# Performance work log

Measured on AMD Instinct MI355X. Metric: run time of the kernel, lower is better.

Reference implementation:

```python
import jax, jax.numpy as jnp
import numpy as np

NUM_NODES = 200000
NUM_LAYERS = 3
EMBED_DIM = 64
NUM_EDGES = 3200000
NUM_PAIRS = 1000000


def setup_inputs() -> dict:
    key = jax.random.key(0)
    k1, k2, k3 = jax.random.split(key, 3)
    emb = jax.random.normal(k1, (NUM_NODES, EMBED_DIM), dtype=jnp.float32)
    alpha = jnp.ones((NUM_LAYERS + 1,), dtype=jnp.float32) * (1.0 / (NUM_LAYERS + 1))
    edge_index = jax.random.randint(k2, (2, NUM_EDGES), 0, NUM_NODES, dtype=jnp.int32)
    edge_label_index = jax.random.randint(k3, (2, NUM_PAIRS), 0, NUM_NODES, dtype=jnp.int32)
    return {"emb": emb, "alpha": alpha, "edge_index": edge_index,
            "edge_label_index": edge_label_index}


def reference(emb, alpha, edge_index, edge_label_index):
    row, col = edge_index[0], edge_index[1]  # source -> target
    # symmetric normalization (gcn_norm without self-loops, as in LGConv)
    ones = jnp.ones((row.shape[0],), dtype=emb.dtype)
    deg = jax.ops.segment_sum(ones, col, num_segments=NUM_NODES)
    dinv = jnp.where(deg > 0, jax.lax.rsqrt(jnp.maximum(deg, 1.0)), 0.0)
    norm = dinv[row] * dinv[col]  # [E]

    x = emb
    out = x * alpha[0]
    for l in range(NUM_LAYERS):
        # gather messages from sources, scale by norm, scatter-add into targets
        msgs = x[row] * norm[:, None]                      # [E, D]
        x = jax.ops.segment_sum(msgs, col, num_segments=NUM_NODES)  # [N, D]
        out = out + x * alpha[l + 1]

    src = out[edge_label_index[0]]  # [P, D]
    dst = out[edge_label_index[1]]  # [P, D]
    return jnp.sum(src * dst, axis=-1)  # [P]
```

## Files before the change

### kernel.cpp

```cpp
#include <hip/hip_runtime.h>
#include <hip/hip_fp16.h>

#define N_NODES 200000
#define N_EDGES 3200000
#define N_PAIRS 1000000
#define DIM 64
#define CAP 48
#define NPB 256
#define NB 782
#define BKTCAP 5120
#define BSTRIDE 16

#define CBITS 11
#define NBC 98
#define BKTCAPA 34816
#define CHUNKA 4096
#define NBLKA ((N_EDGES + CHUNKA - 1) / CHUNKA)
#define BUFB 4400

__global__ void partA_kernel(const int* __restrict__ row, const int* __restrict__ col,
                             int* __restrict__ bktcntA, unsigned* __restrict__ stagingA, int E) {
    __shared__ unsigned buf[CHUNKA];
    __shared__ int cntA[128], offA[128];
    __shared__ int curA[NBC], baseA[NBC];
    int tid = threadIdx.x;
    for (int i = tid; i < 128; i += 256) cntA[i] = 0;
    __syncthreads();
    int start = blockIdx.x * CHUNKA;
    unsigned pk[16];
    int bk[16];
    #pragma unroll
    for (int k = 0; k < 16; ++k) {
        int e = start + k * 256 + tid;
        if (e < E) {
            int c = col[e];
            int r = row[e];
            pk[k] = ((unsigned)(c & 2047) << 18) | (unsigned)r;
            bk[k] = c >> CBITS;
            atomicAdd(&cntA[bk[k]], 1);
        } else bk[k] = -1;
    }
    __syncthreads();
    if (tid < 128) offA[tid] = cntA[tid];
    __syncthreads();
    for (int d = 1; d < 128; d <<= 1) {
        int v = 0;
        if (tid < 128 && tid >= d) v = offA[tid - d];
        __syncthreads();
        if (tid < 128) offA[tid] += v;
        __syncthreads();
    }
    if (tid < NBC) {
        int x = offA[tid] - cntA[tid];
        curA[tid] = x;
        offA[tid] = x;
        baseA[tid] = (cntA[tid] > 0) ? atomicAdd(&bktcntA[tid * BSTRIDE], cntA[tid]) : 0;
    }
    __syncthreads();
    #pragma unroll
    for (int k = 0; k < 16; ++k) {
        if (bk[k] >= 0) {
            int p = atomicAdd(&curA[bk[k]], 1);
            buf[p] = pk[k];
        }
    }
    __syncthreads();
    for (int b = 0; b < NBC; ++b) {
        int n = cntA[b];
        if (n == 0) continue;
        int base = baseA[b];
        if (base + n > BKTCAPA) n = max(0, BKTCAPA - base);
        unsigned* dst = stagingA + (size_t)b * BKTCAPA + base;
        const int o = offA[b];
        for (int i = tid; i < n; i += 256) dst[i] = buf[o + i];
    }
}

__global__ void partB_kernel(const unsigned* __restrict__ stagingA, const int* __restrict__ bktcntA,
                             int* __restrict__ bktcntB, unsigned* __restrict__ stagingB) {
    __shared__ unsigned buf[BUFB];
    __shared__ int cntB[8], offB[8], curB[8], baseB[8];
    int bc = blockIdx.x >> 3;
    int s  = blockIdx.x & 7;
    int tid = threadIdx.x;
    if (tid < 8) cntB[tid] = 0;
    __syncthreads();
    int cnt = min(bktcntA[bc * BSTRIDE], BKTCAPA);
    int slice = (cnt + 7) >> 3;
    int lo = s * slice;
    int hi = min(lo + slice, cnt);
    int n = max(hi - lo, 0);
    const unsigned* src = stagingA + (size_t)bc * BKTCAPA + lo;
    for (int i = tid; i < n; i += 256) atomicAdd(&cntB[src[i] >> 26], 1);
    __syncthreads();
    if (tid == 0) {
        int a = 0;
        for (int b = 0; b < 8; ++b) { offB[b] = a; a += cntB[b]; }
    }
    __syncthreads();
    if (tid < 8) {
        curB[tid] = offB[tid];
        baseB[tid] = (cntB[tid] > 0) ? atomicAdd(&bktcntB[(bc * 8 + tid) * BSTRIDE], cntB[tid]) : 0;
    }
    __syncthreads();
    for (int i = tid; i < n; i += 256) {
        unsigned e = src[i];
        int fb = e >> 26;
        int p = atomicAdd(&curB[fb], 1);
        buf[p] = e & 0x3FFFFFFu;
    }
    __syncthreads();
    for (int b = 0; b < 8; ++b) {
        int m = cntB[b];
        if (m == 0) continue;
        int base = baseB[b];
        if (base + m > BKTCAP) m = max(0, BKTCAP - base);
        unsigned* dst = stagingB + (size_t)(bc * 8 + b) * BKTCAP + base;
        const int o = offB[b];
        for (int i = tid; i < m; i += 256) dst[i] = buf[o + i];
    }
}

__global__ void build_kernel(const unsigned* __restrict__ staging, const int* __restrict__ bktcnt,
                             int* __restrict__ srcrow, int* __restrict__ deg,
                             float* __restrict__ dinv, int N) {
    __shared__ int tile[NPB * CAP];
    __shared__ int cur[NPB];
    int b = blockIdx.x;
    for (int i = threadIdx.x; i < NPB; i += 256) cur[i] = 0;
    __syncthreads();
    int cnt = min(bktcnt[b * BSTRIDE], BKTCAP);
    const unsigned* st = staging + (size_t)b * BKTCAP;
    for (int i = threadIdx.x; i < cnt; i += 256) {
        unsigned packed = st[i];
        int r = packed & 0x3FFFF;
        int cl = packed >> 18;
        int p = atomicAdd(&cur[cl], 1);
        if (p < CAP) tile[cl * CAP + p] = r;
    }
    __syncthreads();
    int nodeBase = b * NPB;
    int nvalid = min(NPB, N - nodeBase);
    for (int i = threadIdx.x; i < nvalid; i += 256) {
        int d = min(cur[i], CAP);
        deg[nodeBase + i] = d;
        dinv[nodeBase + i] = (d > 0) ? rsqrtf((float)d) : 0.0f;
    }
    int tot = nvalid * CAP;
    int* dst = srcrow + (size_t)nodeBase * CAP;
    for (int i = threadIdx.x; i < tot; i += 256) dst[i] = tile[i];
}

__global__ void ewpack_kernel(unsigned int* __restrict__ ew, const int* __restrict__ deg,
                              int total) {
    int s = blockIdx.x * blockDim.x + threadIdx.x;
    if (s >= total) return;
    int n = s / CAP;
    int l = s - n * CAP;
    unsigned int e = 0;
    if (l < deg[n]) {
        int r = (int)ew[s];
        e = (unsigned int)r | ((unsigned int)deg[r] << 18);
    }
    ew[s] = e;
}

__global__ void convert_kernel(const float2* __restrict__ x, __half2* __restrict__ y, int n2) {
    int i = blockIdx.x * blockDim.x + threadIdx.x;
    if (i < n2) {
        float2 v = x[i];
        y[i] = __floats2half2_rn(v.x, v.y);
    }
}

__device__ __forceinline__ float2 h2f(unsigned int u) {
    __half2 h = *(__half2*)&u;
    return __half22float2(h);
}

__global__ void prop_kernel(const uint2* __restrict__ x, const unsigned int* __restrict__ ew,
                            const int* __restrict__ deg, const float* __restrict__ dinv,
                            uint2* __restrict__ xn, int N) {
    __shared__ int2 lds[4][CAP];
    int wv = threadIdx.x >> 6;
    int n = blockIdx.x * 4 + wv;
    int l = threadIdx.x & 63;
    int q = l & 15;
    int quarter = l >> 4;
    int cnt = deg[n];
    if (l < CAP) {
        unsigned int e = ew[(unsigned int)n * CAP + l];
        int id = e & 0x3FFFF;
        int dr = e >> 18;
        float w = dr ? rsqrtf((float)dr) : 0.0f;
        lds[wv][l] = make_int2(id, __float_as_int(w));
    }
    __syncthreads();
    float a0 = 0.f, a1 = 0.f, a2 = 0.f, a3 = 0.f;
    int trips = (cnt + 3) >> 2;
    #pragma unroll 4
    for (int k = 0; k < trips; ++k) {
        int2 e = lds[wv][k * 4 + quarter];
        float w = __int_as_float(e.y);
        uint2 pix = x[(unsigned int)e.x * 16u + q];
        float2 flo = h2f(pix.x);
        float2 fhi = h2f(pix.y);
        a0 += flo.x * w; a1 += flo.y * w;
        a2 += fhi.x * w; a3 += fhi.y * w;
    }
    a0 += __shfl_xor(a0, 16, 64); a1 += __shfl_xor(a1, 16, 64);
    a2 += __shfl_xor(a2, 16, 64); a3 += __shfl_xor(a3, 16, 64);
    a0 += __shfl_xor(a0, 32, 64); a1 += __shfl_xor(a1, 32, 64);
    a2 += __shfl_xor(a2, 32, 64); a3 += __shfl_xor(a3, 32, 64);
    float dn = dinv[n];
    if (quarter == 0) {
        __half2 o01 = __floats2half2_rn(a0 * dn, a1 * dn);
        __half2 o23 = __floats2half2_rn(a2 * dn, a3 * dn);
        uint2 out;
        out.x = *(unsigned int*)&o01;
        out.y = *(unsigned int*)&o23;
        xn[(unsigned int)n * 16u + q] = out;
    }
}

__global__ void prop_final_kernel(const uint2* __restrict__ x, const unsigned int* __restrict__ ew,
                                  const int* __restrict__ deg, const float* __restrict__ dinv,
                                  const uint2* __restrict__ h0, const uint2* __restrict__ h1,
                                  const float* __restrict__ alpha,
                                  uint2* __restrict__ outh, int N) {
    __shared__ int2 lds[4][CAP];
    int wv = threadIdx.x >> 6;
    int n = blockIdx.x * 4 + wv;
    int l = threadIdx.x & 63;
    int q = l & 15;
    int quarter = l >> 4;
    int cnt = deg[n];
    if (l < CAP) {
        unsigned int e = ew[(unsigned int)n * CAP + l];
        int id = e & 0x3FFFF;
        int dr = e >> 18;
        float w = dr ? rsqrtf((float)dr) : 0.0f;
        lds[wv][l] = make_int2(id, __float_as_int(w));
    }
    __syncthreads();
    float a0 = 0.f, a1 = 0.f, a2 = 0.f, a3 = 0.f;
    int trips = (cnt + 3) >> 2;
    #pragma unroll 4
    for (int k = 0; k < trips; ++k) {
        int2 e = lds[wv][k * 4 + quarter];
        float w = __int_as_float(e.y);
        uint2 pix = x[(unsigned int)e.x * 16u + q];
        float2 flo = h2f(pix.x);
        float2 fhi = h2f(pix.y);
        a0 += flo.x * w; a1 += flo.y * w;
        a2 += fhi.x * w; a3 += fhi.y * w;
    }
    a0 += __shfl_xor(a0, 16, 64); a1 += __shfl_xor(a1, 16, 64);
    a2 += __shfl_xor(a2, 16, 64); a3 += __shfl_xor(a3, 16, 64);
    a0 += __shfl_xor(a0, 32, 64); a1 += __shfl_xor(a1, 32, 64);
    a2 += __shfl_xor(a2, 32, 64); a3 += __shfl_xor(a3, 32, 64);
    float dn = dinv[n];
    if (quarter == 0) {
        float al0 = alpha[0], al1 = alpha[1], al2 = alpha[2], al3 = alpha[3];
        unsigned int idx = (unsigned int)n * 16u + q;
        uint2 p0 = h0[idx];
        uint2 p1 = h1[idx];
        uint2 p2 = x[idx];
        float2 f0l = h2f(p0.x), f0h = h2f(p0.y);
        float2 f1l = h2f(p1.x), f1h = h2f(p1.y);
        float2 f2l = h2f(p2.x), f2h = h2f(p2.y);
        float r0 = al0 * f0l.x + al1 * f1l.x + al2 * f2l.x + al3 * (a0 * dn);
        float r1 = al0 * f0l.y + al1 * f1l.y + al2 * f2l.y + al3 * (a1 * dn);
        float r2 = al0 * f0h.x + al1 * f1h.x + al2 * f2h.x + al3 * (a2 * dn);
        float r3 = al0 * f0h.y + al1 * f1h.y + al2 * f2h.y + al3 * (a3 * dn);
        __half2 o01 = __floats2half2_rn(r0, r1);
        __half2 o23 = __floats2half2_rn(r2, r3);
        uint2 out;
        out.x = *(unsigned int*)&o01;
        out.y = *(unsigned int*)&o23;
        outh[idx] = out;
    }
}

__global__ void dot_kernel(const uint2* __restrict__ outh, const int* __restrict__ pa,
                           const int* __restrict__ pb, float* __restrict__ res, int P) {
    int t = blockIdx.x * blockDim.x + threadIdx.x;
    int g = t >> 4;
    int l = threadIdx.x & 15;
    int half = P >> 1;
    if (g >= half) return;
    int p0 = g, p1 = g + half;
    int a0 = pa[p0], b0 = pb[p0];
    int a1 = pa[p1], b1 = pb[p1];
    uint2 ua0 = outh[(size_t)a0 * 16 + l];
    uint2 ub0 = outh[(size_t)b0 * 16 + l];
    uint2 ua1 = outh[(size_t)a1 * 16 + l];
    uint2 ub1 = outh[(size_t)b1 * 16 + l];
    float2 fx0 = h2f(ua0.x), fx1 = h2f(ua0.y);
    float2 fy0 = h2f(ub0.x), fy1 = h2f(ub0.y);
    float s0 = fx0.x * fy0.x + fx0.y * fy0.y + fx1.x * fy1.x + fx1.y * fy1.y;
    float2 fu0 = h2f(ua1.x), fu1 = h2f(ua1.y);
    float2 fv0 = h2f(ub1.x), fv1 = h2f(ub1.y);
    float s1 = fu0.x * fv0.x + fu0.y * fv0.y + fu1.x * fv1.x + fu1.y * fv1.y;
    s0 += __shfl_xor(s0, 1, 64);
    s1 += __shfl_xor(s1, 1, 64);
    s0 += __shfl_xor(s0, 2, 64);
    s1 += __shfl_xor(s1, 2, 64);
    s0 += __shfl_xor(s0, 4, 64);
    s1 += __shfl_xor(s1, 4, 64);
    s0 += __shfl_xor(s0, 8, 64);
    s1 += __shfl_xor(s1, 8, 64);
    if (l == 0) {
        res[p0] = s0;
        res[p1] = s1;
    }
}

extern "C" void kernel_launch(void* const* d_in, const int* in_sizes, int n_in,
                              void* d_out, int out_size, void* d_ws, size_t ws_size,
                              hipStream_t stream) {
    const float* emb   = (const float*)d_in[0];
    const float* alpha = (const float*)d_in[1];
    const int*   ei    = (const int*)d_in[2];
    const int*   eli   = (const int*)d_in[3];
    const int* row = ei;
    const int* col = ei + N_EDGES;
    const int* pa  = eli;
    const int* pb  = eli + N_PAIRS;
    float* res = (float*)d_out;

    const size_t hfeat_bytes = (size_t)N_NODES * DIM * sizeof(__half);
    char* ws = (char*)d_ws;
    size_t off = 0;
    auto alloc = [&](size_t bytes) {
        void* p = ws + off;
        off += (bytes + 255) & ~(size_t)255;
        return p;
    };
    int*      bktcntA  = (int*)alloc((size_t)NBC * BSTRIDE * sizeof(int));
    int*      bktcntB  = (int*)alloc((size_t)NB * BSTRIDE * sizeof(int));
    unsigned* stagingA = (unsigned*)alloc((size_t)NBC * BKTCAPA * sizeof(unsigned));
    unsigned* stagingB = (unsigned*)alloc((size_t)NB * BKTCAP * sizeof(unsigned));
    int*      srcrow   = (int*)alloc((size_t)N_NODES * CAP * sizeof(int));
    int*      deg      = (int*)alloc((size_t)N_NODES * sizeof(int));
    float*    dinv     = (float*)alloc((size_t)N_NODES * sizeof(float));
    __half*   h0       = (__half*)alloc(hfeat_bytes);
    __half*   h1       = (__half*)alloc(hfeat_bytes);
    __half*   h2       = (__half*)alloc(hfeat_bytes);
    __half*   outh     = (__half*)alloc(hfeat_bytes);
    unsigned int* ew = (unsigned int*)srcrow;

    hipMemsetAsync(bktcntA, 0, (size_t)NBC * BSTRIDE * sizeof(int), stream);
    hipMemsetAsync(bktcntB, 0, (size_t)NB * BSTRIDE * sizeof(int), stream);
    partA_kernel<<<NBLKA, 256, 0, stream>>>(row, col, bktcntA, stagingA, N_EDGES);
    partB_kernel<<<NBC * 8, 256, 0, stream>>>(stagingA, bktcntA, bktcntB, stagingB);
    build_kernel<<<NB, 256, 0, stream>>>(stagingB, bktcntB, srcrow, deg, dinv, N_NODES);
    const int total_slots = N_NODES * CAP;
    ewpack_kernel<<<(total_slots + 255) / 256, 256, 0, stream>>>(ew, deg, total_slots);

    const int n2 = N_NODES * DIM / 2;
    convert_kernel<<<(n2 + 255) / 256, 256, 0, stream>>>((const float2*)emb, (__half2*)h0, n2);

    const int prop_grid = N_NODES / 4;
    prop_kernel<<<prop_grid, 256, 0, stream>>>((const uint2*)h0, ew, deg, dinv, (uint2*)h1, N_NODES);
    prop_kernel<<<prop_grid, 256, 0, stream>>>((const uint2*)h1, ew, deg, dinv, (uint2*)h2, N_NODES);
    prop_final_kernel<<<prop_grid, 256, 0, stream>>>((const uint2*)h2, ew, deg, dinv,
                                                     (const uint2*)h0, (const uint2*)h1,
                                                     alpha, (uint2*)outh, N_NODES);

    dot_kernel<<<((size_t)(N_PAIRS / 2) * 16 + 255) / 256, 256, 0, stream>>>(
        (const uint2*)outh, pa, pb, res, N_PAIRS);
}
```

Baseline: 378.2 us.

## Drop second partition pass; build kernel filters coarse buckets directly

Removes the partB kernel and the second staging buffer. Each build block now scans its whole coarse bucket from stagingA (about 32K entries) and keeps only the entries whose sub-bucket bits match its own index. This saves a kernel launch, a memset and one full write-then-read of the staged edge list through global memory. In exchange, each coarse bucket is read eight times (once by each of its eight build blocks), so build does about eight times the read and filter work.

```diff
diff --git a/kernel.cpp b/kernel.cpp
--- a/kernel.cpp
+++ b/kernel.cpp
@@ -8,7 +8,6 @@
 #define CAP 48
 #define NPB 256
 #define NB 782
-#define BKTCAP 5120
 #define BSTRIDE 16
 
 #define CBITS 11
@@ -16,7 +15,6 @@
 #define BKTCAPA 34816
 #define CHUNKA 4096
 #define NBLKA ((N_EDGES + CHUNKA - 1) / CHUNKA)
-#define BUFB 4400
 
 __global__ void partA_kernel(const int* __restrict__ row, const int* __restrict__ col,
                              int* __restrict__ bktcntA, unsigned* __restrict__ stagingA, int E) {
@@ -76,67 +74,25 @@
     }
 }
 
-__global__ void partB_kernel(const unsigned* __restrict__ stagingA, const int* __restrict__ bktcntA,
-                             int* __restrict__ bktcntB, unsigned* __restrict__ stagingB) {
-    __shared__ unsigned buf[BUFB];
-    __shared__ int cntB[8], offB[8], curB[8], baseB[8];
-    int bc = blockIdx.x >> 3;
-    int s  = blockIdx.x & 7;
-    int tid = threadIdx.x;
-    if (tid < 8) cntB[tid] = 0;
-    __syncthreads();
-    int cnt = min(bktcntA[bc * BSTRIDE], BKTCAPA);
-    int slice = (cnt + 7) >> 3;
-    int lo = s * slice;
-    int hi = min(lo + slice, cnt);
-    int n = max(hi - lo, 0);
-    const unsigned* src = stagingA + (size_t)bc * BKTCAPA + lo;
-    for (int i = tid; i < n; i += 256) atomicAdd(&cntB[src[i] >> 26], 1);
-    __syncthreads();
-    if (tid == 0) {
-        int a = 0;
-        for (int b = 0; b < 8; ++b) { offB[b] = a; a += cntB[b]; }
-    }
-    __syncthreads();
-    if (tid < 8) {
-        curB[tid] = offB[tid];
-        baseB[tid] = (cntB[tid] > 0) ? atomicAdd(&bktcntB[(bc * 8 + tid) * BSTRIDE], cntB[tid]) : 0;
-    }
-    __syncthreads();
-    for (int i = tid; i < n; i += 256) {
-        unsigned e = src[i];
-        int fb = e >> 26;
-        int p = atomicAdd(&curB[fb], 1);
-        buf[p] = e & 0x3FFFFFFu;
-    }
-    __syncthreads();
-    for (int b = 0; b < 8; ++b) {
-        int m = cntB[b];
-        if (m == 0) continue;
-        int base = baseB[b];
-        if (base + m > BKTCAP) m = max(0, BKTCAP - base);
-        unsigned* dst = stagingB + (size_t)(bc * 8 + b) * BKTCAP + base;
-        const int o = offB[b];
-        for (int i = tid; i < m; i += 256) dst[i] = buf[o + i];
-    }
-}
-
-__global__ void build_kernel(const unsigned* __restrict__ staging, const int* __restrict__ bktcnt,
+__global__ void build_kernel(const unsigned* __restrict__ stagingA, const int* __restrict__ bktcntA,
                              int* __restrict__ srcrow, int* __restrict__ deg,
                              float* __restrict__ dinv, int N) {
     __shared__ int tile[NPB * CAP];
     __shared__ int cur[NPB];
     int b = blockIdx.x;
+    int bc = b >> 3;
+    unsigned fb = (unsigned)(b & 7);
     for (int i = threadIdx.x; i < NPB; i += 256) cur[i] = 0;
     __syncthreads();
-    int cnt = min(bktcnt[b * BSTRIDE], BKTCAP);
-    const unsigned* st = staging + (size_t)b * BKTCAP;
+    int cnt = min(bktcntA[bc * BSTRIDE], BKTCAPA);
+    const unsigned* st = stagingA + (size_t)bc * BKTCAPA;
     for (int i = threadIdx.x; i < cnt; i += 256) {
-        unsigned packed = st[i];
-        int r = packed & 0x3FFFF;
-        int cl = packed >> 18;
-        int p = atomicAdd(&cur[cl], 1);
-        if (p < CAP) tile[cl * CAP + p] = r;
+        unsigned e = st[i];
+        if ((e >> 26) == fb) {
+            int cl = (e >> 18) & 255;
+            int p = atomicAdd(&cur[cl], 1);
+            if (p < CAP) tile[cl * CAP + p] = (int)(e & 0x3FFFFu);
+        }
     }
     __syncthreads();
     int nodeBase = b * NPB;
@@ -338,9 +294,7 @@
         return p;
     };
     int*      bktcntA  = (int*)alloc((size_t)NBC * BSTRIDE * sizeof(int));
-    int*      bktcntB  = (int*)alloc((size_t)NB * BSTRIDE * sizeof(int));
     unsigned* stagingA = (unsigned*)alloc((size_t)NBC * BKTCAPA * sizeof(unsigned));
-    unsigned* stagingB = (unsigned*)alloc((size_t)NB * BKTCAP * sizeof(unsigned));
     int*      srcrow   = (int*)alloc((size_t)N_NODES * CAP * sizeof(int));
     int*      deg      = (int*)alloc((size_t)N_NODES * sizeof(int));
     float*    dinv     = (float*)alloc((size_t)N_NODES * sizeof(float));
@@ -351,10 +305,8 @@
     unsigned int* ew = (unsigned int*)srcrow;
 
     hipMemsetAsync(bktcntA, 0, (size_t)NBC * BSTRIDE * sizeof(int), stream);
-    hipMemsetAsync(bktcntB, 0, (size_t)NB * BSTRIDE * sizeof(int), stream);
     partA_kernel<<<NBLKA, 256, 0, stream>>>(row, col, bktcntA, stagingA, N_EDGES);
-    partB_kernel<<<NBC * 8, 256, 0, stream>>>(stagingA, bktcntA, bktcntB, stagingB);
-    build_kernel<<<NB, 256, 0, stream>>>(stagingB, bktcntB, srcrow, deg, dinv, N_NODES);
+    build_kernel<<<NB, 256, 0, stream>>>(stagingA, bktcntA, srcrow, deg, dinv, N_NODES);
     const int total_slots = N_NODES * CAP;
     ewpack_kernel<<<(total_slots + 255) / 256, 256, 0, stream>>>(ew, deg, total_slots);
 
```

Result: slower. 431.8 us (+14.2%).
